# Optimization experiments

Hardware: AMD Instinct MI355X
Metric: run time of the kernel (lower is better)

Reference implementation:

```python
import jax, jax.numpy as jnp
import numpy as np

N, D, K, P, A = 16384, 256, 32, 64, 5
H, KD, NPT, FACT = 8, 32, 8, 2
RBF_BINS, RBF_MAX, REL_CLIP = 16, 10.0, 32


def _norm(v, eps=1e-6):
    return v * jax.lax.rsqrt(jnp.square(v).sum(-1, keepdims=True) + eps)


def extract_frames(pos):
    # pos: [N, A, 3]; backbone atoms 0=N, 1=CA, 2=C (Gram-Schmidt AF-style frame)
    n, ca, c = pos[:, 0], pos[:, 1], pos[:, 2]
    e1 = _norm(c - ca)
    u = n - ca
    e2 = _norm(u - (u * e1).sum(-1, keepdims=True) * e1)
    e3 = jnp.cross(e1, e2)
    R = jnp.stack([e1, e2, e3], axis=-1)  # [N,3,3], columns = frame axes
    t = ca
    local = jnp.einsum('nji,naj->nai', R, pos - t[:, None])  # R^T (p - t)
    return R, t, local


def distance_rbf(d):
    centers = jnp.linspace(0.0, RBF_MAX, RBF_BINS)
    sigma = RBF_MAX / RBF_BINS
    return jnp.exp(-jnp.square((d[..., None] - centers) / sigma))


def layer_norm(x, scale, offset, eps=1e-5):
    mu = x.mean(-1, keepdims=True)
    var = jnp.square(x - mu).mean(-1, keepdims=True)
    return (x - mu) * jax.lax.rsqrt(var + eps) * scale + offset


def setup_inputs() -> dict:
    key = jax.random.key(0)
    ks = jax.random.split(key, 20)
    f32 = jnp.float32
    rnd = lambda i, shape, s=0.02: jax.random.normal(ks[i], shape, f32) * s
    inp = {}
    inp['local'] = jax.random.normal(ks[0], (N, D), f32)
    inp['pos'] = jax.random.normal(ks[1], (N, A, 3), f32) * 3.0
    inp['neighbours'] = jax.random.randint(ks[2], (N, K), 0, N, jnp.int32)
    inp['resi'] = jnp.arange(N, dtype=jnp.int32) % 512
    inp['chain'] = jnp.arange(N, dtype=jnp.int32) // 2048
    inp['batch'] = jnp.arange(N, dtype=jnp.int32) // 4096
    inp['update_mask'] = jnp.ones((N, 1), bool)
    inp['mask'] = jnp.ones((N,), bool)
    FIN = A * 3 + A * RBF_BINS
    FPAIR = A * 3 + A * RBF_BINS + (2 * REL_CLIP + 1) + 2
    FOUT = H * KD + H * P + H * NPT * 3 + H * NPT
    inp['w_in'] = rnd(3, (FIN, D))
    inp['w_pair'] = rnd(4, (FPAIR, P))
    inp['b_pair'] = jnp.zeros((P,), f32)
    inp['ln1_s'] = jnp.ones((D,), f32); inp['ln1_o'] = jnp.zeros((D,), f32)
    inp['wq'] = rnd(5, (D, H * KD)); inp['wk'] = rnd(6, (D, H * KD)); inp['wv'] = rnd(7, (D, H * KD))
    inp['wqp'] = rnd(8, (D, H * NPT * 3)); inp['wkp'] = rnd(9, (D, H * NPT * 3)); inp['wvp'] = rnd(10, (D, H * NPT * 3))
    inp['wb'] = rnd(11, (P, H))
    inp['gamma'] = jnp.ones((H,), f32)
    inp['wo'] = rnd(12, (FOUT, D)); inp['bo'] = jnp.zeros((D,), f32)
    inp['ln2_s'] = jnp.ones((D,), f32); inp['ln2_o'] = jnp.zeros((D,), f32)
    DH = D * FACT
    inp['wg'] = rnd(13, (D, DH)); inp['wvm'] = rnd(14, (D, DH)); inp['wom'] = rnd(15, (DH, D))
    inp['ln3_s'] = jnp.ones((D,), f32); inp['ln3_o'] = jnp.zeros((D,), f32)
    inp['wpos'] = rnd(16, (D, A * 3))
    return inp


def reference(local, pos, w_in, w_pair, b_pair, ln1_s, ln1_o, wq, wk, wv, wqp, wkp, wvp,
              wb, gamma, wo, bo, ln2_s, ln2_o, wg, wvm, wom, ln3_s, ln3_o, wpos,
              neighbours, resi, chain, batch, update_mask, mask):
    n_res = local.shape[0]
    kk = neighbours.shape[1]
    R, t, local_pos = extract_frames(pos)  # [N,3,3], [N,3], [N,A,3]
    # --- geometric input features ---
    dloc = jnp.sqrt(jnp.square(local_pos).sum(-1) + 1e-12)
    feat = jnp.concatenate([_norm(local_pos).reshape(n_res, -1),
                            distance_rbf(dloc).reshape(n_res, -1)], axis=-1)
    local = local + feat @ w_in
    # --- pair features over kNN edges ---
    idx = jnp.clip(neighbours, 0, n_res - 1)
    pos_j = pos[idx]  # [N,K,A,3]
    rel = jnp.einsum('nji,nkaj->nkai', R, pos_j - t[:, None, None])  # neighbour atoms in frame i
    dij = jnp.sqrt(jnp.square(rel).sum(-1) + 1e-12)  # [N,K,A]
    dirs = rel / (dij[..., None] + 1e-6)
    rp = jnp.clip(resi[idx] - resi[:, None], -REL_CLIP, REL_CLIP) + REL_CLIP
    rp_oh = jax.nn.one_hot(rp, 2 * REL_CLIP + 1, dtype=local.dtype)
    same_chain = (chain[idx] == chain[:, None])[..., None].astype(local.dtype)
    same_batch = (batch[idx] == batch[:, None])[..., None].astype(local.dtype)
    pf = jnp.concatenate([dirs.reshape(n_res, kk, -1), distance_rbf(dij).reshape(n_res, kk, -1),
                          rp_oh, same_chain, same_batch], axis=-1)
    pair = jax.nn.gelu(pf @ w_pair + b_pair)  # [N,K,P]
    pair_mask = mask[:, None] & mask[idx] & (neighbours >= 0) & (batch[idx] == batch[:, None])
    # --- sparse invariant point attention ---
    x = layer_norm(local, ln1_s, ln1_o)
    q = (x @ wq).reshape(n_res, H, KD)
    k = (x @ wk).reshape(n_res, H, KD)
    v = (x @ wv).reshape(n_res, H, KD)
    to_glob = lambda pts: jnp.einsum('nij,nhpj->nhpi', R, pts) + t[:, None, None]
    qp = to_glob((x @ wqp).reshape(n_res, H, NPT, 3))
    kp = to_glob((x @ wkp).reshape(n_res, H, NPT, 3))
    vp = to_glob((x @ wvp).reshape(n_res, H, NPT, 3))
    qk = jnp.einsum('nhd,nkhd->nkh', q, k[idx]) / np.float32(np.sqrt(KD))
    d2 = jnp.square(qp[:, None] - kp[idx]).sum(-1).sum(-1)  # [N,K,H]
    wc = np.float32(np.sqrt(2.0 / (9.0 * NPT)))
    wl = np.float32(np.sqrt(1.0 / 3.0))
    logits = wl * (qk + pair @ wb - 0.5 * wc * jax.nn.softplus(gamma) * d2)
    logits = jnp.where(pair_mask[..., None], logits, -1e9)
    att = jax.nn.softmax(logits, axis=1)
    att = jnp.where(pair_mask[..., None], att, 0.0)
    o_s = jnp.einsum('nkh,nkhd->nhd', att, v[idx]).reshape(n_res, -1)
    o_pt = jnp.einsum('nkh,nkhpi->nhpi', att, vp[idx])
    o_pt = jnp.einsum('nji,nhpj->nhpi', R, o_pt - t[:, None, None])  # back to local frame
    o_n = jnp.sqrt(jnp.square(o_pt).sum(-1) + 1e-8)
    o_pr = jnp.einsum('nkh,nkc->nhc', att, pair).reshape(n_res, -1)
    ipa = jnp.concatenate([o_s, o_pr, o_pt.reshape(n_res, -1), o_n.reshape(n_res, -1)], -1) @ wo + bo
    local = local + ipa
    # --- gated MLP ---
    x = layer_norm(local, ln2_s, ln2_o)
    local = local + (jax.nn.gelu(x @ wg) * (x @ wvm)) @ wom
    # --- equivariant position update (scale = 1.0) ---
    x = layer_norm(local, ln3_s, ln3_o)
    new_lp = local_pos + (x @ wpos).reshape(n_res, A, 3)
    new_pos = jnp.einsum('nij,naj->nai', R, new_lp) + t[:, None]
    pos = jnp.where(update_mask[..., None], new_pos, pos)
    return local, pos
```

## Files before the change

### kernel.cpp

```cpp
#include <hip/hip_runtime.h>
#include <hip/hip_bf16.h>
#include <math.h>

#define DMODEL 256
#define KNB 32
#define NHEAD 8
#define FIN 95
#define FPD 95
#define KPAD 104
#define FOUT 1024
#define DHID 512

typedef __hip_bfloat16 bf16;
typedef __attribute__((ext_vector_type(8))) short short8;
typedef __attribute__((ext_vector_type(4))) float floatx4;

__device__ inline float B2F(bf16 x) { return __bfloat162float(x); }
__device__ inline bf16 F2B(float x) { return __float2bfloat16(x); }
__device__ inline unsigned short f2bs(float x) {
    bf16 h = __float2bfloat16(x);
    return *reinterpret_cast<unsigned short*>(&h);
}
__device__ inline float bs2f(short s) {
    return __uint_as_float(((unsigned)(unsigned short)s) << 16);
}

__device__ inline float gelu_t(float x) {
    return 0.5f * x * (1.f + tanhf(0.7978845608028654f * (x + 0.044715f * x * x * x)));
}

#define OFF_WALL 0
#define OFF_WO   344064
#define OFF_WG   606208
#define OFF_WVM  737280
#define OFF_WOM  868352
#define OFF_WP   999424
#define OFF_WIN  1006080
#define WT_TOTAL 1032704

__global__ __launch_bounds__(256) void kT(const float* __restrict__ wq, const float* __restrict__ wk,
                                          const float* __restrict__ wv, const float* __restrict__ wqp,
                                          const float* __restrict__ wkp, const float* __restrict__ wvp,
                                          const float* __restrict__ wo, const float* __restrict__ wg,
                                          const float* __restrict__ wvm, const float* __restrict__ wom,
                                          const float* __restrict__ w_pair, const float* __restrict__ w_in,
                                          unsigned short* __restrict__ wt) {
    int stride = gridDim.x * 256;
    for (int e = blockIdx.x * 256 + threadIdx.x; e < WT_TOTAL; e += stride) {
        float v;
        if (e < OFF_WO) {
            int n = e >> 8, k = e & 255;
            if (n < 256) v = wq[k * 256 + n];
            else if (n < 512) v = wk[k * 256 + n - 256];
            else if (n < 768) v = wv[k * 256 + n - 512];
            else if (n < 960) v = wqp[k * 192 + n - 768];
            else if (n < 1152) v = wkp[k * 192 + n - 960];
            else v = wvp[k * 192 + n - 1152];
        } else if (e < OFF_WG) {
            int u = e - OFF_WO; int n = u >> 10, k = u & 1023;
            v = wo[k * 256 + n];
        } else if (e < OFF_WVM) {
            int u = e - OFF_WG; int n = u >> 8, k = u & 255;
            v = wg[k * 512 + n];
        } else if (e < OFF_WOM) {
            int u = e - OFF_WVM; int n = u >> 8, k = u & 255;
            v = wvm[k * 512 + n];
        } else if (e < OFF_WP) {
            int u = e - OFF_WOM; int n = u >> 9, k = u & 511;
            v = wom[k * 256 + n];
        } else if (e < OFF_WIN) {
            int u = e - OFF_WP; int n = u / KPAD, k = u % KPAD;
            v = (k < FPD) ? w_pair[k * 64 + n] : 0.f;
        } else {
            int u = e - OFF_WIN; int n = u / KPAD, k = u % KPAD;
            v = (k < FIN) ? w_in[k * 256 + n] : 0.f;
        }
        wt[e] = f2bs(v);
    }
}

__global__ __launch_bounds__(256) void kA1(const float* __restrict__ pos,
                                           float* __restrict__ Rw,
                                           float* __restrict__ lpw,
                                           unsigned short* __restrict__ featb) {
    int tid = threadIdx.x;
    int res = tid >> 5, lt = tid & 31;
    int ri = blockIdx.x * 8 + res;
    const float* pp = pos + (size_t)ri * 15;
    float nx = pp[0], ny = pp[1], nz = pp[2];
    float cax = pp[3], cay = pp[4], caz = pp[5];
    float cx = pp[6], cy = pp[7], cz = pp[8];
    float e1x = cx - cax, e1y = cy - cay, e1z = cz - caz;
    float inv = rsqrtf(e1x * e1x + e1y * e1y + e1z * e1z + 1e-6f);
    e1x *= inv; e1y *= inv; e1z *= inv;
    float ux = nx - cax, uy = ny - cay, uz = nz - caz;
    float d = ux * e1x + uy * e1y + uz * e1z;
    float wx = ux - d * e1x, wy = uy - d * e1y, wz = uz - d * e1z;
    inv = rsqrtf(wx * wx + wy * wy + wz * wz + 1e-6f);
    float e2x = wx * inv, e2y = wy * inv, e2z = wz * inv;
    float e3x = e1y * e2z - e1z * e2y;
    float e3y = e1z * e2x - e1x * e2z;
    float e3z = e1x * e2y - e1y * e2x;
    float R[9] = {e1x, e2x, e3x, e1y, e2y, e3y, e1z, e2z, e3z};

    __shared__ float lpS[8][15];
    __shared__ float ddS[8][5], dinvS[8][5];

    if (lt < 9) Rw[(size_t)ri * 9 + lt] = R[lt];
    if (lt < 15) {
        int a = lt / 3, ii = lt % 3;
        float px = pp[a * 3 + 0] - cax, py = pp[a * 3 + 1] - cay, pz = pp[a * 3 + 2] - caz;
        float v = R[0 * 3 + ii] * px + R[1 * 3 + ii] * py + R[2 * 3 + ii] * pz;
        lpS[res][lt] = v;
        lpw[(size_t)ri * 15 + lt] = v;
    }
    __syncthreads();
    if (lt < 5) {
        float s = lpS[res][lt * 3] * lpS[res][lt * 3] + lpS[res][lt * 3 + 1] * lpS[res][lt * 3 + 1] +
                  lpS[res][lt * 3 + 2] * lpS[res][lt * 3 + 2];
        ddS[res][lt] = sqrtf(s + 1e-12f);
        dinvS[res][lt] = rsqrtf(s + 1e-6f);
    }
    __syncthreads();
    for (int e = lt; e < KPAD; e += 32) {
        float v;
        if (e < 15) v = lpS[res][e] * dinvS[res][e / 3];
        else if (e < 95) {
            int u = e - 15, a = u >> 4, b = u & 15;
            float z = (ddS[res][a] - (float)b * (10.f / 15.f)) * (1.f / 0.625f);
            v = expf(-z * z);
        } else v = 0.f;
        featb[(size_t)ri * KPAD + e] = f2bs(v);
    }
}

__global__ __launch_bounds__(256) void kB(const float* __restrict__ local,
                                          const unsigned short* __restrict__ featb,
                                          const float* __restrict__ ln1_s,
                                          const float* __restrict__ ln1_o,
                                          const unsigned short* __restrict__ wAllT,
                                          const unsigned short* __restrict__ w_inT,
                                          float* __restrict__ dlocal,
                                          bf16* __restrict__ qbh, bf16* __restrict__ kvb,
                                          bf16* __restrict__ qpl, bf16* __restrict__ kpl,
                                          bf16* __restrict__ vpl) {
    int r0 = blockIdx.x * 32;
    int tid = threadIdx.x;
    __shared__ __align__(16) unsigned short featA[32 * KPAD];
    __shared__ __align__(16) unsigned short xbf[32 * 264];
    __shared__ float statsS[32 * 4];

    {
        const short8* src = reinterpret_cast<const short8*>(featb + (size_t)r0 * KPAD);
        short8* dst = reinterpret_cast<short8*>(featA);
        for (int c = tid; c < 32 * KPAD / 8; c += 256) dst[c] = src[c];
    }
    __syncthreads();

    int lane = tid & 63, w = tid >> 6;
    int mtile = w & 1, par = w >> 1;
    int m = lane & 15, quad = lane >> 4;

    short8 fa[3];
#pragma unroll
    for (int ks = 0; ks < 3; ks++)
        fa[ks] = *reinterpret_cast<const short8*>(&featA[(mtile * 16 + m) * KPAD + ks * 32 + quad * 8]);
    float lupv[8][4];
#pragma unroll
    for (int j = 0; j < 8; j++) {
        int nt = par + 2 * j;
        floatx4 c = {0.f, 0.f, 0.f, 0.f};
        const short8* bp = reinterpret_cast<const short8*>(w_inT + (size_t)(nt * 16 + m) * KPAD);
#pragma unroll
        for (int ks = 0; ks < 3; ks++)
            c = __builtin_amdgcn_mfma_f32_16x16x32_bf16(fa[ks], bp[ks * 4 + quad], c, 0, 0, 0);
        int col = nt * 16 + m;
#pragma unroll
        for (int r = 0; r < 4; r++) {
            int row = mtile * 16 + quad * 4 + r;
            float lv = local[(size_t)(r0 + row) * 256 + col] + c[r];
            lupv[j][r] = lv;
            dlocal[(size_t)(r0 + row) * 256 + col] = lv;
        }
    }
    {
        float s[4] = {0.f, 0.f, 0.f, 0.f}, ss[4] = {0.f, 0.f, 0.f, 0.f};
#pragma unroll
        for (int j = 0; j < 8; j++)
#pragma unroll
            for (int r = 0; r < 4; r++) { s[r] += lupv[j][r]; ss[r] += lupv[j][r] * lupv[j][r]; }
#pragma unroll
        for (int mask = 1; mask < 16; mask <<= 1)
#pragma unroll
            for (int r = 0; r < 4; r++) { s[r] += __shfl_xor(s[r], mask); ss[r] += __shfl_xor(ss[r], mask); }
        if (m == 0) {
#pragma unroll
            for (int r = 0; r < 4; r++) {
                int row = mtile * 16 + quad * 4 + r;
                statsS[row * 4 + par * 2 + 0] = s[r];
                statsS[row * 4 + par * 2 + 1] = ss[r];
            }
        }
    }
    __syncthreads();
    {
        float mu[4], rs_[4];
#pragma unroll
        for (int r = 0; r < 4; r++) {
            int row = mtile * 16 + quad * 4 + r;
            float S = statsS[row * 4 + 0] + statsS[row * 4 + 2];
            float SS = statsS[row * 4 + 1] + statsS[row * 4 + 3];
            float m_ = S * (1.f / 256.f);
            mu[r] = m_;
            rs_[r] = rsqrtf(SS * (1.f / 256.f) - m_ * m_ + 1e-5f);
        }
#pragma unroll
        for (int j = 0; j < 8; j++) {
            int col = (par + 2 * j) * 16 + m;
            float g = ln1_s[col], o = ln1_o[col];
#pragma unroll
            for (int r = 0; r < 4; r++) {
                int row = mtile * 16 + quad * 4 + r;
                xbf[row * 264 + col] = f2bs((lupv[j][r] - mu[r]) * rs_[r] * g + o);
            }
        }
    }
    __syncthreads();

    short8 afr[8];
#pragma unroll
    for (int ks = 0; ks < 8; ks++)
        afr[ks] = *reinterpret_cast<const short8*>(&xbf[(mtile * 16 + m) * 264 + ks * 32 + quad * 8]);
    for (int nt = par; nt < 84; nt += 2) {
        floatx4 c = {0.f, 0.f, 0.f, 0.f};
        const short8* bp = reinterpret_cast<const short8*>(wAllT + (size_t)(nt * 16 + m) * 256);
#pragma unroll
        for (int ks = 0; ks < 8; ks++)
            c = __builtin_amdgcn_mfma_f32_16x16x32_bf16(afr[ks], bp[ks * 4 + quad], c, 0, 0, 0);
        int colg = nt * 16 + m;
        bf16* O; int c0, ncol;
        if (colg < 256)       { O = qbh; c0 = colg;        ncol = 256; }
        else if (colg < 768)  { O = kvb; c0 = colg - 256;  ncol = 512; }
        else if (colg < 960)  { O = qpl; c0 = colg - 768;  ncol = 192; }
        else if (colg < 1152) { O = kpl; c0 = colg - 960;  ncol = 192; }
        else                  { O = vpl; c0 = colg - 1152; ncol = 192; }
#pragma unroll
        for (int r = 0; r < 4; r++) {
            int rg = r0 + mtile * 16 + quad * 4 + r;
            O[(size_t)rg * ncol + c0] = F2B(c[r]);
        }
    }
}

__global__ __launch_bounds__(256) void kP(const bf16* __restrict__ qpl,
                                          const bf16* __restrict__ kpl,
                                          const bf16* __restrict__ vpl,
                                          const float* __restrict__ Rw,
                                          const float* __restrict__ pos,
                                          float* __restrict__ qpg,
                                          float* __restrict__ kvpg) {
    int r0 = blockIdx.x * 4;
    int tid = threadIdx.x;
    for (int u = tid; u < 4 * 192; u += 256) {
        int r = u / 192, e = u % 192, hp = e / 3, ii = e % 3;
        int ri = r0 + r;
        float R0 = Rw[(size_t)ri * 9 + ii * 3 + 0];
        float R1 = Rw[(size_t)ri * 9 + ii * 3 + 1];
        float R2 = Rw[(size_t)ri * 9 + ii * 3 + 2];
        float tt = pos[(size_t)ri * 15 + 3 + ii];
        size_t base = (size_t)ri * 192 + hp * 3;
        qpg[(size_t)ri * 192 + e] = R0 * B2F(qpl[base]) + R1 * B2F(qpl[base + 1]) + R2 * B2F(qpl[base + 2]) + tt;
        kvpg[(size_t)ri * 384 + e] = R0 * B2F(kpl[base]) + R1 * B2F(kpl[base + 1]) + R2 * B2F(kpl[base + 2]) + tt;
        kvpg[(size_t)ri * 384 + 192 + e] = R0 * B2F(vpl[base]) + R1 * B2F(vpl[base + 1]) + R2 * B2F(vpl[base + 2]) + tt;
    }
}

__global__ __launch_bounds__(256) void kC(const float* __restrict__ pos,
                                          const int* __restrict__ nbr,
                                          const int* __restrict__ resi,
                                          const int* __restrict__ chain,
                                          const int* __restrict__ batch,
                                          const int* __restrict__ mask,
                                          const float* __restrict__ Rw,
                                          const float* __restrict__ w_pair,
                                          const unsigned short* __restrict__ wT,
                                          const float* __restrict__ b_pair,
                                          const float* __restrict__ wbm,
                                          const float* __restrict__ gamma,
                                          const bf16* __restrict__ qbh,
                                          const bf16* __restrict__ kvb,
                                          const float* __restrict__ qpg,
                                          const float* __restrict__ kvpg,
                                          bf16* __restrict__ ipab,
                                          int N) {
    int i = blockIdx.x;
    int tid = threadIdx.x;
    __shared__ __align__(16) float qS[256];
    __shared__ __align__(16) float qpS[192];
    __shared__ __align__(16) unsigned short pfA[KNB * KPAD];
    __shared__ __align__(16) float pairS[KNB][68];
    __shared__ __align__(16) float wbmS[NHEAD][68];
    __shared__ float spS[NHEAD];
    __shared__ float lg[KNB * NHEAD];
    __shared__ float optg[192];
    __shared__ float ipaS[FOUT];
    __shared__ int idxS[KNB], rpS[KNB], scS[KNB], sbS[KNB], pmS[KNB];

    float R[9];
#pragma unroll
    for (int u = 0; u < 9; u++) R[u] = Rw[(size_t)i * 9 + u];
    float t0 = pos[(size_t)i * 15 + 3];
    float t1 = pos[(size_t)i * 15 + 4];
    float t2 = pos[(size_t)i * 15 + 5];

    qS[tid] = B2F(qbh[(size_t)i * 256 + tid]);
    if (tid < 192) qpS[tid] = qpg[(size_t)i * 192 + tid];
    if (tid < KNB) {
        int nb = nbr[(size_t)i * KNB + tid];
        int j = min(max(nb, 0), N - 1);
        idxS[tid] = j;
        int rp = resi[j] - resi[i];
        rp = min(max(rp, -32), 32) + 32;
        rpS[tid] = rp;
        scS[tid] = (chain[j] == chain[i]) ? 1 : 0;
        sbS[tid] = (batch[j] == batch[i]) ? 1 : 0;
        pmS[tid] = (mask[i] != 0 && mask[j] != 0 && nb >= 0 && batch[j] == batch[i]) ? 1 : 0;
    }
    __syncthreads();
    for (int u = tid; u < 512; u += 256) {
        int h = u & 7, c = u >> 3;
        wbmS[h][c] = wbm[c * 8 + h];
    }
    if (tid >= 192 && tid < 200) spS[tid - 192] = log1pf(expf(gamma[tid - 192]));
    if (tid < 160) {
        int kk = tid & 31, a = tid >> 5;
        int j = idxS[kk];
        const float* pj = pos + (size_t)j * 15 + a * 3;
        float px = pj[0] - t0, py = pj[1] - t1, pz = pj[2] - t2;
        float r0_ = R[0] * px + R[3] * py + R[6] * pz;
        float r1_ = R[1] * px + R[4] * py + R[7] * pz;
        float r2_ = R[2] * px + R[5] * py + R[8] * pz;
        float s = r0_ * r0_ + r1_ * r1_ + r2_ * r2_;
        float dij = sqrtf(s + 1e-12f);
        float di = 1.f / (dij + 1e-6f);
        pfA[kk * KPAD + a * 3 + 0] = f2bs(r0_ * di);
        pfA[kk * KPAD + a * 3 + 1] = f2bs(r1_ * di);
        pfA[kk * KPAD + a * 3 + 2] = f2bs(r2_ * di);
        for (int b = 0; b < 16; b++) {
            float z = (dij - (float)b * (10.f / 15.f)) * (1.f / 0.625f);
            pfA[kk * KPAD + 15 + a * 16 + b] = f2bs(expf(-z * z));
        }
    }
    if (tid < KNB) pfA[tid * KPAD + FPD] = 0;
    __syncthreads();

    {
        int lane = tid & 63;
        int wv = tid >> 6;
        int n0 = wv * 16;
        int mrow = lane & 15;
        int quad = lane >> 4;
        floatx4 c0 = {0.f, 0.f, 0.f, 0.f};
        floatx4 c1 = {0.f, 0.f, 0.f, 0.f};
#pragma unroll
        for (int ks = 0; ks < 3; ks++) {
            int k0 = ks * 32 + quad * 8;
            short8 a0 = *reinterpret_cast<const short8*>(&pfA[mrow * KPAD + k0]);
            short8 a1 = *reinterpret_cast<const short8*>(&pfA[(16 + mrow) * KPAD + k0]);
            short8 bb = *reinterpret_cast<const short8*>(&wT[(n0 + mrow) * KPAD + k0]);
            c0 = __builtin_amdgcn_mfma_f32_16x16x32_bf16(a0, bb, c0, 0, 0, 0);
            c1 = __builtin_amdgcn_mfma_f32_16x16x32_bf16(a1, bb, c1, 0, 0, 0);
        }
        int col = n0 + mrow;
        float bp = b_pair[col];
        float w160 = w_pair[160 * 64 + col];
        float w161 = w_pair[161 * 64 + col];
#pragma unroll
        for (int mt = 0; mt < 2; mt++) {
            floatx4 cc = mt ? c1 : c0;
#pragma unroll
            for (int r = 0; r < 4; r++) {
                int row = mt * 16 + quad * 4 + r;
                float s = cc[r] + bp + w_pair[(95 + rpS[row]) * 64 + col] +
                          (scS[row] ? w160 : 0.f) + (sbS[row] ? w161 : 0.f);
                pairS[row][col] = gelu_t(s);
            }
        }
    }
    __syncthreads();

    {
        int kk = tid >> 3, h = tid & 7;
        int j = idxS[kk];
        float qk = 0.f;
        const short8* kj8 = reinterpret_cast<const short8*>(kvb + (size_t)j * 512 + h * 32);
        const floatx4* qh4 = reinterpret_cast<const floatx4*>(qS + h * 32);
#pragma unroll
        for (int e = 0; e < 4; e++) {
            short8 kv = kj8[e];
            floatx4 qa = qh4[2 * e], qb = qh4[2 * e + 1];
            qk += qa[0] * bs2f(kv[0]) + qa[1] * bs2f(kv[1]) + qa[2] * bs2f(kv[2]) + qa[3] * bs2f(kv[3]) +
                  qb[0] * bs2f(kv[4]) + qb[1] * bs2f(kv[5]) + qb[2] * bs2f(kv[6]) + qb[3] * bs2f(kv[7]);
        }
        qk *= 0.17677669529663687f;
        float d2 = 0.f;
        const floatx4* kp4 = reinterpret_cast<const floatx4*>(kvpg + (size_t)j * 384 + h * 24);
        const floatx4* qp4 = reinterpret_cast<const floatx4*>(qpS + h * 24);
#pragma unroll
        for (int e = 0; e < 6; e++) {
            floatx4 kv = kp4[e], qv = qp4[e];
#pragma unroll
            for (int q = 0; q < 4; q++) {
                float df = qv[q] - kv[q];
                d2 += df * df;
            }
        }
        float pb = 0.f;
        const floatx4* ps4 = reinterpret_cast<const floatx4*>(&pairS[kk][0]);
        const floatx4* wb4 = reinterpret_cast<const floatx4*>(&wbmS[h][0]);
#pragma unroll
        for (int e = 0; e < 16; e++) {
            floatx4 pv = ps4[e], wv4 = wb4[e];
            pb += pv[0] * wv4[0] + pv[1] * wv4[1] + pv[2] * wv4[2] + pv[3] * wv4[3];
        }
        float lgt = 0.5773502691896258f * (qk + pb - (1.f / 12.f) * spS[h] * d2);
        lg[kk * 8 + h] = pmS[kk] ? lgt : -1e9f;
    }
    __syncthreads();
    if (tid < 64) {
        int h = tid >> 3, sub = tid & 7;
        float m = -INFINITY;
        float lv[4];
#pragma unroll
        for (int q = 0; q < 4; q++) {
            lv[q] = lg[(sub + 8 * q) * 8 + h];
            m = fmaxf(m, lv[q]);
        }
#pragma unroll
        for (int mk = 1; mk < 8; mk <<= 1) m = fmaxf(m, __shfl_xor(m, mk));
        float s = 0.f, ex[4];
#pragma unroll
        for (int q = 0; q < 4; q++) { ex[q] = expf(lv[q] - m); s += ex[q]; }
#pragma unroll
        for (int mk = 1; mk < 8; mk <<= 1) s += __shfl_xor(s, mk);
        float invs = 1.f / s;
#pragma unroll
        for (int q = 0; q < 4; q++) {
            int kk = sub + 8 * q;
            lg[kk * 8 + h] = pmS[kk] ? ex[q] * invs : 0.f;
        }
    }
    __syncthreads();
    {
        int h = tid >> 5, d = tid & 31;
        float s = 0.f;
        for (int kk = 0; kk < KNB; kk++)
            s += lg[kk * 8 + h] * B2F(kvb[(size_t)idxS[kk] * 512 + 256 + h * 32 + d]);
        ipaS[h * 32 + d] = s;
    }
    for (int u = tid; u < 512; u += 256) {
        int h = u >> 6, c = u & 63;
        float s = 0.f;
        for (int kk = 0; kk < KNB; kk++) s += lg[kk * 8 + h] * pairS[kk][c];
        ipaS[256 + u] = s;
    }
    if (tid < 192) {
        int h = tid / 24;
        float s = 0.f;
        for (int kk = 0; kk < KNB; kk++)
            s += lg[kk * 8 + h] * kvpg[(size_t)idxS[kk] * 384 + 192 + tid];
        optg[tid] = s;
    }
    __syncthreads();
    if (tid < 192) {
        int hp = tid / 3, ii = tid % 3;
        float v0 = optg[hp * 3 + 0] - t0, v1 = optg[hp * 3 + 1] - t1, v2 = optg[hp * 3 + 2] - t2;
        ipaS[768 + tid] = R[0 + ii] * v0 + R[3 + ii] * v1 + R[6 + ii] * v2;
    }
    __syncthreads();
    if (tid < 64) {
        float a0 = ipaS[768 + tid * 3], a1 = ipaS[768 + tid * 3 + 1], a2 = ipaS[768 + tid * 3 + 2];
        ipaS[960 + tid] = sqrtf(a0 * a0 + a1 * a1 + a2 * a2 + 1e-8f);
    }
    __syncthreads();
    for (int u = tid; u < FOUT; u += 256) ipab[(size_t)i * FOUT + u] = F2B(ipaS[u]);
}

__global__ __launch_bounds__(256) void kDE(const bf16* __restrict__ ipab,
                                           const unsigned short* __restrict__ woT,
                                           const float* __restrict__ bo,
                                           const float* __restrict__ ln2_s,
                                           const float* __restrict__ ln2_o,
                                           const unsigned short* __restrict__ wgT,
                                           const unsigned short* __restrict__ wvmT,
                                           const unsigned short* __restrict__ womT,
                                           float* __restrict__ dlocal) {
    int r0 = blockIdx.x * 32;
    int tid = threadIdx.x;
    __shared__ __align__(16) unsigned short xbf[32 * 264];
    __shared__ __align__(16) unsigned short hbf[32 * 520];
    __shared__ float statsS[32 * 4];
    int lane = tid & 63, w = tid >> 6;
    int mtile = w & 1, par = w >> 1, m = lane & 15, quad = lane >> 4;

    floatx4 l2[8];
#pragma unroll
    for (int j = 0; j < 8; j++) l2[j] = {0.f, 0.f, 0.f, 0.f};
    const short8* arow = reinterpret_cast<const short8*>(ipab + (size_t)(r0 + mtile * 16 + m) * 1024);
    for (int ks = 0; ks < 32; ks++) {
        short8 a = arow[ks * 4 + quad];
#pragma unroll
        for (int j = 0; j < 8; j++) {
            int nt = par + 2 * j;
            const short8* bp = reinterpret_cast<const short8*>(woT + (size_t)(nt * 16 + m) * 1024);
            l2[j] = __builtin_amdgcn_mfma_f32_16x16x32_bf16(a, bp[ks * 4 + quad], l2[j], 0, 0, 0);
        }
    }
#pragma unroll
    for (int j = 0; j < 8; j++) {
        int colg = (par + 2 * j) * 16 + m;
        float bov = bo[colg];
#pragma unroll
        for (int r = 0; r < 4; r++) {
            int row = mtile * 16 + quad * 4 + r;
            l2[j][r] += dlocal[(size_t)(r0 + row) * 256 + colg] + bov;
        }
    }
    {
        float s[4] = {0.f, 0.f, 0.f, 0.f}, ss[4] = {0.f, 0.f, 0.f, 0.f};
#pragma unroll
        for (int j = 0; j < 8; j++)
#pragma unroll
            for (int r = 0; r < 4; r++) { s[r] += l2[j][r]; ss[r] += l2[j][r] * l2[j][r]; }
#pragma unroll
        for (int mask = 1; mask < 16; mask <<= 1)
#pragma unroll
            for (int r = 0; r < 4; r++) { s[r] += __shfl_xor(s[r], mask); ss[r] += __shfl_xor(ss[r], mask); }
        if (m == 0) {
#pragma unroll
            for (int r = 0; r < 4; r++) {
                int row = mtile * 16 + quad * 4 + r;
                statsS[row * 4 + par * 2 + 0] = s[r];
                statsS[row * 4 + par * 2 + 1] = ss[r];
            }
        }
    }
    __syncthreads();
    {
        float mu[4], rs_[4];
#pragma unroll
        for (int r = 0; r < 4; r++) {
            int row = mtile * 16 + quad * 4 + r;
            float S = statsS[row * 4 + 0] + statsS[row * 4 + 2];
            float SS = statsS[row * 4 + 1] + statsS[row * 4 + 3];
            float m_ = S * (1.f / 256.f);
            mu[r] = m_;
            rs_[r] = rsqrtf(SS * (1.f / 256.f) - m_ * m_ + 1e-5f);
        }
#pragma unroll
        for (int j = 0; j < 8; j++) {
            int colg = (par + 2 * j) * 16 + m;
            float g = ln2_s[colg], o = ln2_o[colg];
#pragma unroll
            for (int r = 0; r < 4; r++) {
                int row = mtile * 16 + quad * 4 + r;
                xbf[row * 264 + colg] = f2bs((l2[j][r] - mu[r]) * rs_[r] * g + o);
            }
        }
    }
    __syncthreads();
    short8 afr[8];
#pragma unroll
    for (int ks = 0; ks < 8; ks++)
        afr[ks] = *reinterpret_cast<const short8*>(&xbf[(mtile * 16 + m) * 264 + ks * 32 + quad * 8]);
    for (int nt = par; nt < 32; nt += 2) {
        floatx4 cg = {0.f, 0.f, 0.f, 0.f};
        floatx4 cv = {0.f, 0.f, 0.f, 0.f};
        const short8* bg = reinterpret_cast<const short8*>(wgT + (size_t)(nt * 16 + m) * 256);
        const short8* bv = reinterpret_cast<const short8*>(wvmT + (size_t)(nt * 16 + m) * 256);
#pragma unroll
        for (int ks = 0; ks < 8; ks++) {
            cg = __builtin_amdgcn_mfma_f32_16x16x32_bf16(afr[ks], bg[ks * 4 + quad], cg, 0, 0, 0);
            cv = __builtin_amdgcn_mfma_f32_16x16x32_bf16(afr[ks], bv[ks * 4 + quad], cv, 0, 0, 0);
        }
#pragma unroll
        for (int r = 0; r < 4; r++) {
            int row = mtile * 16 + quad * 4 + r;
            hbf[row * 520 + nt * 16 + m] = f2bs(gelu_t(cg[r]) * cv[r]);
        }
    }
    __syncthreads();
    floatx4 acc[8];
#pragma unroll
    for (int j = 0; j < 8; j++) acc[j] = {0.f, 0.f, 0.f, 0.f};
    for (int ks = 0; ks < 16; ks++) {
        short8 a = *reinterpret_cast<const short8*>(&hbf[(mtile * 16 + m) * 520 + ks * 32 + quad * 8]);
#pragma unroll
        for (int j = 0; j < 8; j++) {
            int nt = par + 2 * j;
            const short8* bp = reinterpret_cast<const short8*>(womT + (size_t)(nt * 16 + m) * 512);
            acc[j] = __builtin_amdgcn_mfma_f32_16x16x32_bf16(a, bp[ks * 4 + quad], acc[j], 0, 0, 0);
        }
    }
#pragma unroll
    for (int j = 0; j < 8; j++) {
        int colg = (par + 2 * j) * 16 + m;
#pragma unroll
        for (int r = 0; r < 4; r++) {
            int row = mtile * 16 + quad * 4 + r;
            dlocal[(size_t)(r0 + row) * 256 + colg] = l2[j][r] + acc[j][r];
        }
    }
}

__global__ __launch_bounds__(256) void kF(const float* __restrict__ dlocal,
                                          const float* __restrict__ ln3_s,
                                          const float* __restrict__ ln3_o,
                                          const float* __restrict__ wpos,
                                          const float* __restrict__ lpw,
                                          const float* __restrict__ Rw,
                                          const float* __restrict__ pos,
                                          const int* __restrict__ umask,
                                          float* __restrict__ outp) {
    int tid = threadIdx.x;
    int r = tid >> 5, lt = tid & 31;
    int ri = blockIdx.x * 8 + r;
    __shared__ float x3S[8][256];
    __shared__ float nlS[8][15];
    {
        const floatx4* src = reinterpret_cast<const floatx4*>(dlocal + (size_t)ri * 256 + lt * 8);
        floatx4 v0 = src[0], v1 = src[1];
        float s = 0.f, ss = 0.f;
#pragma unroll
        for (int q = 0; q < 4; q++) {
            s += v0[q] + v1[q];
            ss += v0[q] * v0[q] + v1[q] * v1[q];
        }
#pragma unroll
        for (int mask = 1; mask < 32; mask <<= 1) { s += __shfl_xor(s, mask); ss += __shfl_xor(ss, mask); }
        float mu = s * (1.f / 256.f);
        float var = ss * (1.f / 256.f) - mu * mu;
        float rs = rsqrtf(var + 1e-5f);
#pragma unroll
        for (int q = 0; q < 4; q++) {
            int f0 = lt * 8 + q, f1 = lt * 8 + 4 + q;
            x3S[r][f0] = (v0[q] - mu) * rs * ln3_s[f0] + ln3_o[f0];
            x3S[r][f1] = (v1[q] - mu) * rs * ln3_s[f1] + ln3_o[f1];
        }
    }
    __syncthreads();
    {
        int g = tid >> 5, sub = tid & 31;
        for (int out = g; out < 120; out += 8) {
            int rr = out / 15, e = out % 15;
            float partial = 0.f;
#pragma unroll
            for (int i2 = 0; i2 < 8; i2++) {
                int f = sub + 32 * i2;
                partial += x3S[rr][f] * wpos[f * 15 + e];
            }
#pragma unroll
            for (int mask = 1; mask < 32; mask <<= 1) partial += __shfl_xor(partial, mask);
            if (sub == 0) nlS[rr][e] = lpw[(size_t)(blockIdx.x * 8 + rr) * 15 + e] + partial;
        }
    }
    __syncthreads();
    if (tid < 120) {
        int rr = tid / 15, e = tid % 15;
        int rj = blockIdx.x * 8 + rr;
        int a2 = e / 3, ii = e % 3;
        float R0 = Rw[(size_t)rj * 9 + ii * 3 + 0];
        float R1 = Rw[(size_t)rj * 9 + ii * 3 + 1];
        float R2 = Rw[(size_t)rj * 9 + ii * 3 + 2];
        float tt = pos[(size_t)rj * 15 + 3 + ii];
        float np = R0 * nlS[rr][a2 * 3 + 0] + R1 * nlS[rr][a2 * 3 + 1] + R2 * nlS[rr][a2 * 3 + 2] + tt;
        float old = pos[(size_t)rj * 15 + e];
        outp[(size_t)rj * 15 + e] = (umask[rj] != 0) ? np : old;
    }
}

extern "C" void kernel_launch(void* const* d_in, const int* in_sizes, int n_in,
                              void* d_out, int out_size, void* d_ws, size_t ws_size,
                              hipStream_t stream) {
    static const int map_dict[31] = {0, 1, 2, 3, 4, 5, 6, 7, 8, 9, 10, 11, 12, 13, 14, 15,
                                     16, 17, 18, 19, 20, 21, 22, 23, 24, 25, 26, 27, 28, 29, 30};
    static const int map_sig[31] = {0, 1, 25, 26, 27, 28, 29, 30, 2, 3, 4, 5, 6, 7, 8, 9,
                                    10, 11, 12, 13, 14, 15, 16, 17, 18, 19, 20, 21, 22, 23, 24};
    const int* M = (in_sizes[2] == FIN * DMODEL) ? map_sig : map_dict;

    const float* local = (const float*)d_in[M[0]];
    const float* pos = (const float*)d_in[M[1]];
    const int* nbr = (const int*)d_in[M[2]];
    const int* resi = (const int*)d_in[M[3]];
    const int* chain = (const int*)d_in[M[4]];
    const int* batch = (const int*)d_in[M[5]];
    const int* umask = (const int*)d_in[M[6]];
    const int* mask = (const int*)d_in[M[7]];
    const float* w_in = (const float*)d_in[M[8]];
    const float* w_pair = (const float*)d_in[M[9]];
    const float* b_pair = (const float*)d_in[M[10]];
    const float* ln1_s = (const float*)d_in[M[11]];
    const float* ln1_o = (const float*)d_in[M[12]];
    const float* wq = (const float*)d_in[M[13]];
    const float* wk = (const float*)d_in[M[14]];
    const float* wv = (const float*)d_in[M[15]];
    const float* wqp = (const float*)d_in[M[16]];
    const float* wkp = (const float*)d_in[M[17]];
    const float* wvp = (const float*)d_in[M[18]];
    const float* wbm = (const float*)d_in[M[19]];
    const float* gamma = (const float*)d_in[M[20]];
    const float* wo = (const float*)d_in[M[21]];
    const float* bo = (const float*)d_in[M[22]];
    const float* ln2_s = (const float*)d_in[M[23]];
    const float* ln2_o = (const float*)d_in[M[24]];
    const float* wg = (const float*)d_in[M[25]];
    const float* wvm = (const float*)d_in[M[26]];
    const float* wom = (const float*)d_in[M[27]];
    const float* ln3_s = (const float*)d_in[M[28]];
    const float* ln3_o = (const float*)d_in[M[29]];
    const float* wpos = (const float*)d_in[M[30]];

    int N = in_sizes[0] / DMODEL;

    float* out_local = (float*)d_out;
    float* out_pos = out_local + (size_t)N * DMODEL;

    char* wsb = (char*)d_ws;
    float* Rw = (float*)wsb;   wsb += (size_t)N * 9 * 4;
    float* lpw = (float*)wsb;  wsb += (size_t)N * 15 * 4;
    bf16* qbh = (bf16*)wsb;    wsb += (size_t)N * 256 * 2;
    bf16* kvb = (bf16*)wsb;    wsb += (size_t)N * 512 * 2;
    bf16* qpl = (bf16*)wsb;    wsb += (size_t)N * 192 * 2;
    bf16* kpl = (bf16*)wsb;    wsb += (size_t)N * 192 * 2;
    bf16* vpl = (bf16*)wsb;    wsb += (size_t)N * 192 * 2;
    bf16* ipab = (bf16*)wsb;   wsb += (size_t)N * 1024 * 2;
    float* qpg = (float*)wsb;  wsb += (size_t)N * 192 * 4;
    float* kvpg = (float*)wsb; wsb += (size_t)N * 384 * 4;
    unsigned short* featb = (unsigned short*)wsb; wsb += (size_t)N * KPAD * 2;
    unsigned short* wtrans = (unsigned short*)wsb; wsb += (size_t)WT_TOTAL * 2;
    unsigned short* wAllT = wtrans + OFF_WALL;
    unsigned short* woT   = wtrans + OFF_WO;
    unsigned short* wgT   = wtrans + OFF_WG;
    unsigned short* wvmT  = wtrans + OFF_WVM;
    unsigned short* womT  = wtrans + OFF_WOM;
    unsigned short* wpT   = wtrans + OFF_WP;
    unsigned short* winT  = wtrans + OFF_WIN;

    dim3 blk(256);
    hipLaunchKernelGGL(kT, dim3(512), blk, 0, stream, wq, wk, wv, wqp, wkp, wvp,
                       wo, wg, wvm, wom, w_pair, w_in, wtrans);
    hipLaunchKernelGGL(kA1, dim3(N / 8), blk, 0, stream, pos, Rw, lpw, featb);
    hipLaunchKernelGGL(kB, dim3(N / 32), blk, 0, stream, local, featb, ln1_s, ln1_o, wAllT, winT,
                       out_local, qbh, kvb, qpl, kpl, vpl);
    hipLaunchKernelGGL(kP, dim3(N / 4), blk, 0, stream, qpl, kpl, vpl, Rw, pos, qpg, kvpg);
    hipLaunchKernelGGL(kC, dim3(N), blk, 0, stream, pos, nbr, resi, chain, batch, mask, Rw,
                       w_pair, wpT, b_pair, wbm, gamma, qbh, kvb, qpg, kvpg, ipab, N);
    hipLaunchKernelGGL(kDE, dim3(N / 32), blk, 0, stream, ipab, woT, bo, ln2_s, ln2_o,
                       wgT, wvmT, womT, out_local);
    hipLaunchKernelGGL(kF, dim3(N / 8), blk, 0, stream, out_local, ln3_s, ln3_o, wpos, lpw, Rw, pos,
                       umask, out_pos);
}
```

Baseline: 673.7 us.

## Use MFMA for attention aggregation and pair bias in IPA kernel

The per-residue attention kernel now stages neighbour values, centred value points and pair features transposed in shared memory as bf16. The attention-weighted sums over neighbours and the pair-bias projection become MFMA matrix multiplies instead of scalar loops over global memory. It also swaps in faster exp/gelu approximations, reuses shared buffers through a union, and adds a bf16 copy of wb to the weight-transpose kernel. This lowers precision for the value aggregation and adds LDS transpose traffic and a correction for the all-masked case.

```diff
diff --git a/kernel.cpp b/kernel.cpp
--- a/kernel.cpp
+++ b/kernel.cpp
@@ -10,6 +10,8 @@
 #define KPAD 104
 #define FOUT 1024
 #define DHID 512
+#define BTS 36
+#define PRS 72
 
 typedef __hip_bfloat16 bf16;
 typedef __attribute__((ext_vector_type(8))) short short8;
@@ -27,6 +29,12 @@
 
 __device__ inline float gelu_t(float x) {
     return 0.5f * x * (1.f + tanhf(0.7978845608028654f * (x + 0.044715f * x * x * x)));
+}
+
+__device__ inline float gelu_f(float x) {
+    float u = 1.5957691216057308f * x * (1.f + 0.044715f * x * x);
+    float t = 1.f - 2.f / (1.f + __expf(u));
+    return 0.5f * x * (1.f + t);
 }
 
 #define OFF_WALL 0
@@ -36,7 +44,8 @@
 #define OFF_WOM  868352
 #define OFF_WP   999424
 #define OFF_WIN  1006080
-#define WT_TOTAL 1032704
+#define OFF_WBM  1032704
+#define WT_TOTAL 1033728
 
 __global__ __launch_bounds__(256) void kT(const float* __restrict__ wq, const float* __restrict__ wk,
                                           const float* __restrict__ wv, const float* __restrict__ wqp,
@@ -44,6 +53,7 @@
                                           const float* __restrict__ wo, const float* __restrict__ wg,
                                           const float* __restrict__ wvm, const float* __restrict__ wom,
                                           const float* __restrict__ w_pair, const float* __restrict__ w_in,
+                                          const float* __restrict__ wbm,
                                           unsigned short* __restrict__ wt) {
     int stride = gridDim.x * 256;
     for (int e = blockIdx.x * 256 + threadIdx.x; e < WT_TOTAL; e += stride) {
@@ -71,9 +81,12 @@
         } else if (e < OFF_WIN) {
             int u = e - OFF_WP; int n = u / KPAD, k = u % KPAD;
             v = (k < FPD) ? w_pair[k * 64 + n] : 0.f;
-        } else {
+        } else if (e < OFF_WBM) {
             int u = e - OFF_WIN; int n = u / KPAD, k = u % KPAD;
             v = (k < FIN) ? w_in[k * 256 + n] : 0.f;
+        } else {
+            int u = e - OFF_WBM; int n = u >> 6, k = u & 63;
+            v = (n < NHEAD) ? wbm[k * 8 + n] : 0.f;
         }
         wt[e] = f2bs(v);
     }
@@ -285,7 +298,7 @@
                                           const float* __restrict__ w_pair,
                                           const unsigned short* __restrict__ wT,
                                           const float* __restrict__ b_pair,
-                                          const float* __restrict__ wbm,
+                                          const unsigned short* __restrict__ wbmT,
                                           const float* __restrict__ gamma,
                                           const bf16* __restrict__ qbh,
                                           const bf16* __restrict__ kvb,
@@ -295,16 +308,19 @@
                                           int N) {
     int i = blockIdx.x;
     int tid = threadIdx.x;
+    __shared__ __align__(16) unsigned short BigT[512 * BTS];
+    __shared__ __align__(16) unsigned short pairR[32 * PRS];
+    __shared__ __align__(16) unsigned short attb[16 * 40];
     __shared__ __align__(16) float qS[256];
     __shared__ __align__(16) float qpS[192];
-    __shared__ __align__(16) unsigned short pfA[KNB * KPAD];
-    __shared__ __align__(16) float pairS[KNB][68];
-    __shared__ __align__(16) float wbmS[NHEAD][68];
+    __shared__ __align__(16) float pbS[256];
     __shared__ float spS[NHEAD];
-    __shared__ float lg[KNB * NHEAD];
-    __shared__ float optg[192];
-    __shared__ float ipaS[FOUT];
+    __shared__ int anyS;
     __shared__ int idxS[KNB], rpS[KNB], scS[KNB], sbS[KNB], pmS[KNB];
+    __shared__ __align__(16) union UShare {
+        unsigned short pfA[32 * KPAD];
+        struct { float ipaS[FOUT]; float optg[192]; } o;
+    } uS;
 
     float R[9];
 #pragma unroll
@@ -315,6 +331,7 @@
 
     qS[tid] = B2F(qbh[(size_t)i * 256 + tid]);
     if (tid < 192) qpS[tid] = qpg[(size_t)i * 192 + tid];
+    if (tid < NHEAD) spS[tid] = log1pf(expf(gamma[tid]));
     if (tid < KNB) {
         int nb = nbr[(size_t)i * KNB + tid];
         int j = min(max(nb, 0), N - 1);
@@ -327,11 +344,10 @@
         pmS[tid] = (mask[i] != 0 && mask[j] != 0 && nb >= 0 && batch[j] == batch[i]) ? 1 : 0;
     }
     __syncthreads();
-    for (int u = tid; u < 512; u += 256) {
-        int h = u & 7, c = u >> 3;
-        wbmS[h][c] = wbm[c * 8 + h];
-    }
-    if (tid >= 192 && tid < 200) spS[tid - 192] = log1pf(expf(gamma[tid - 192]));
+    if (tid < 64) {
+        unsigned long long b = __ballot((tid < KNB) && (pmS[tid] != 0));
+        if (tid == 0) anyS = (b != 0ULL) ? 1 : 0;
+    }
     if (tid < 160) {
         int kk = tid & 31, a = tid >> 5;
         int j = idxS[kk];
@@ -343,15 +359,15 @@
         float s = r0_ * r0_ + r1_ * r1_ + r2_ * r2_;
         float dij = sqrtf(s + 1e-12f);
         float di = 1.f / (dij + 1e-6f);
-        pfA[kk * KPAD + a * 3 + 0] = f2bs(r0_ * di);
-        pfA[kk * KPAD + a * 3 + 1] = f2bs(r1_ * di);
-        pfA[kk * KPAD + a * 3 + 2] = f2bs(r2_ * di);
+        uS.pfA[kk * KPAD + a * 3 + 0] = f2bs(r0_ * di);
+        uS.pfA[kk * KPAD + a * 3 + 1] = f2bs(r1_ * di);
+        uS.pfA[kk * KPAD + a * 3 + 2] = f2bs(r2_ * di);
         for (int b = 0; b < 16; b++) {
             float z = (dij - (float)b * (10.f / 15.f)) * (1.f / 0.625f);
-            pfA[kk * KPAD + 15 + a * 16 + b] = f2bs(expf(-z * z));
-        }
-    }
-    if (tid < KNB) pfA[tid * KPAD + FPD] = 0;
+            uS.pfA[kk * KPAD + 15 + a * 16 + b] = f2bs(__expf(-z * z));
+        }
+    }
+    if (tid < KNB) uS.pfA[tid * KPAD + FPD] = 0;
     __syncthreads();
 
     {
@@ -365,8 +381,8 @@
 #pragma unroll
         for (int ks = 0; ks < 3; ks++) {
             int k0 = ks * 32 + quad * 8;
-            short8 a0 = *reinterpret_cast<const short8*>(&pfA[mrow * KPAD + k0]);
-            short8 a1 = *reinterpret_cast<const short8*>(&pfA[(16 + mrow) * KPAD + k0]);
+            short8 a0 = *reinterpret_cast<const short8*>(&uS.pfA[mrow * KPAD + k0]);
+            short8 a1 = *reinterpret_cast<const short8*>(&uS.pfA[(16 + mrow) * KPAD + k0]);
             short8 bb = *reinterpret_cast<const short8*>(&wT[(n0 + mrow) * KPAD + k0]);
             c0 = __builtin_amdgcn_mfma_f32_16x16x32_bf16(a0, bb, c0, 0, 0, 0);
             c1 = __builtin_amdgcn_mfma_f32_16x16x32_bf16(a1, bb, c1, 0, 0, 0);
@@ -383,7 +399,60 @@
                 int row = mt * 16 + quad * 4 + r;
                 float s = cc[r] + bp + w_pair[(95 + rpS[row]) * 64 + col] +
                           (scS[row] ? w160 : 0.f) + (sbS[row] ? w161 : 0.f);
-                pairS[row][col] = gelu_t(s);
+                unsigned short gb = f2bs(gelu_f(s));
+                pairR[row * PRS + col] = gb;
+                BigT[(448 + col) * BTS + row] = gb;
+            }
+        }
+    }
+    __syncthreads();
+
+    {
+        int kk = tid & 31, seg = tid >> 5;
+        int j = idxS[kk];
+        {
+            const short8* src = reinterpret_cast<const short8*>(kvb + (size_t)j * 512 + 256 + seg * 32);
+            short8 v0 = src[0], v1 = src[1], v2 = src[2], v3 = src[3];
+#pragma unroll
+            for (int c = 0; c < 8; c++) BigT[(seg * 32 + c) * BTS + kk] = (unsigned short)v0[c];
+#pragma unroll
+            for (int c = 0; c < 8; c++) BigT[(seg * 32 + 8 + c) * BTS + kk] = (unsigned short)v1[c];
+#pragma unroll
+            for (int c = 0; c < 8; c++) BigT[(seg * 32 + 16 + c) * BTS + kk] = (unsigned short)v2[c];
+#pragma unroll
+            for (int c = 0; c < 8; c++) BigT[(seg * 32 + 24 + c) * BTS + kk] = (unsigned short)v3[c];
+        }
+        {
+            const floatx4* src = reinterpret_cast<const floatx4*>(kvpg + (size_t)j * 384 + 192 + seg * 24);
+            floatx4 f[6];
+#pragma unroll
+            for (int g = 0; g < 6; g++) f[g] = src[g];
+            float tv[3] = {t0, t1, t2};
+#pragma unroll
+            for (int g = 0; g < 6; g++)
+#pragma unroll
+                for (int c2 = 0; c2 < 4; c2++) {
+                    int x = g * 4 + c2;
+                    float val = f[g][c2] - tv[x % 3];
+                    BigT[(256 + seg * 24 + x) * BTS + kk] = f2bs(val);
+                }
+        }
+    }
+    {
+        int w = tid >> 6;
+        if (w < 2) {
+            int lane = tid & 63, la = lane & 15, quad = lane >> 4;
+            floatx4 c = {0.f, 0.f, 0.f, 0.f};
+#pragma unroll
+            for (int ks = 0; ks < 2; ks++) {
+                short8 a = *reinterpret_cast<const short8*>(&pairR[(w * 16 + la) * PRS + ks * 32 + quad * 8]);
+                short8 b = *reinterpret_cast<const short8*>(wbmT + la * 64 + ks * 32 + quad * 8);
+                c = __builtin_amdgcn_mfma_f32_16x16x32_bf16(a, b, c, 0, 0, 0);
+            }
+            if (la < NHEAD) {
+#pragma unroll
+                for (int r = 0; r < 4; r++)
+                    pbS[(w * 16 + quad * 4 + r) * 8 + la] = c[r];
             }
         }
     }
@@ -415,75 +484,95 @@
                 d2 += df * df;
             }
         }
-        float pb = 0.f;
-        const floatx4* ps4 = reinterpret_cast<const floatx4*>(&pairS[kk][0]);
-        const floatx4* wb4 = reinterpret_cast<const floatx4*>(&wbmS[h][0]);
-#pragma unroll
-        for (int e = 0; e < 16; e++) {
-            floatx4 pv = ps4[e], wv4 = wb4[e];
-            pb += pv[0] * wv4[0] + pv[1] * wv4[1] + pv[2] * wv4[2] + pv[3] * wv4[3];
-        }
+        float pb = pbS[kk * 8 + h];
         float lgt = 0.5773502691896258f * (qk + pb - (1.f / 12.f) * spS[h] * d2);
-        lg[kk * 8 + h] = pmS[kk] ? lgt : -1e9f;
-    }
-    __syncthreads();
+        pbS[kk * 8 + h] = pmS[kk] ? lgt : -1e9f;
+    }
+    __syncthreads();
+
     if (tid < 64) {
         int h = tid >> 3, sub = tid & 7;
         float m = -INFINITY;
         float lv[4];
 #pragma unroll
         for (int q = 0; q < 4; q++) {
-            lv[q] = lg[(sub + 8 * q) * 8 + h];
+            lv[q] = pbS[(sub + 8 * q) * 8 + h];
             m = fmaxf(m, lv[q]);
         }
 #pragma unroll
         for (int mk = 1; mk < 8; mk <<= 1) m = fmaxf(m, __shfl_xor(m, mk));
         float s = 0.f, ex[4];
 #pragma unroll
-        for (int q = 0; q < 4; q++) { ex[q] = expf(lv[q] - m); s += ex[q]; }
+        for (int q = 0; q < 4; q++) { ex[q] = __expf(lv[q] - m); s += ex[q]; }
 #pragma unroll
         for (int mk = 1; mk < 8; mk <<= 1) s += __shfl_xor(s, mk);
         float invs = 1.f / s;
 #pragma unroll
         for (int q = 0; q < 4; q++) {
             int kk = sub + 8 * q;
-            lg[kk * 8 + h] = pmS[kk] ? ex[q] * invs : 0.f;
-        }
-    }
-    __syncthreads();
-    {
-        int h = tid >> 5, d = tid & 31;
-        float s = 0.f;
-        for (int kk = 0; kk < KNB; kk++)
-            s += lg[kk * 8 + h] * B2F(kvb[(size_t)idxS[kk] * 512 + 256 + h * 32 + d]);
-        ipaS[h * 32 + d] = s;
-    }
-    for (int u = tid; u < 512; u += 256) {
-        int h = u >> 6, c = u & 63;
-        float s = 0.f;
-        for (int kk = 0; kk < KNB; kk++) s += lg[kk * 8 + h] * pairS[kk][c];
-        ipaS[256 + u] = s;
-    }
-    if (tid < 192) {
-        int h = tid / 24;
-        float s = 0.f;
-        for (int kk = 0; kk < KNB; kk++)
-            s += lg[kk * 8 + h] * kvpg[(size_t)idxS[kk] * 384 + 192 + tid];
-        optg[tid] = s;
-    }
-    __syncthreads();
+            float a = pmS[kk] ? ex[q] * invs : 0.f;
+            attb[h * 40 + kk] = f2bs(a);
+        }
+    } else if (tid < 128) {
+        int t2 = tid - 64;
+        int h2 = 8 + (t2 >> 3);
+        int k0 = (t2 & 7) * 4;
+#pragma unroll
+        for (int q = 0; q < 4; q++) attb[h2 * 40 + k0 + q] = 0;
+    }
+    __syncthreads();
+
+    {
+        int lane = tid & 63, w = tid >> 6;
+        int la = lane & 15, quad = lane >> 4;
+        short8 af = *reinterpret_cast<const short8*>(&attb[la * 40 + quad * 8]);
+        float* oB = uS.o.ipaS;
+#pragma unroll
+        for (int n8 = 0; n8 < 8; n8++) {
+            int nt = w * 8 + n8;
+            int colg = nt * 16 + la;
+            union { short8 s; unsigned long long u[2]; } bb;
+            const unsigned long long* bp = reinterpret_cast<const unsigned long long*>(&BigT[colg * BTS + quad * 8]);
+            bb.u[0] = bp[0]; bb.u[1] = bp[1];
+            floatx4 z = {0.f, 0.f, 0.f, 0.f};
+            floatx4 d = __builtin_amdgcn_mfma_f32_16x16x32_bf16(af, bb.s, z, 0, 0, 0);
+            if (quad < 2) {
+                if (colg < 448) {
+                    int h_req, dst;
+                    if (colg < 256) { h_req = colg >> 5; dst = (h_req << 5) + (colg & 31); }
+                    else            { int e = colg - 256; h_req = e / 24; dst = 1024 + e; }
+                    if ((h_req >> 2) == quad) {
+#pragma unroll
+                        for (int r = 0; r < 4; r++)
+                            if ((h_req & 3) == r) oB[dst] = d[r];
+                    }
+                } else {
+                    int c = colg - 448;
+#pragma unroll
+                    for (int r = 0; r < 4; r++)
+                        oB[256 + (quad * 4 + r) * 64 + c] = d[r];
+                }
+            }
+        }
+    }
+    __syncthreads();
+
     if (tid < 192) {
         int hp = tid / 3, ii = tid % 3;
-        float v0 = optg[hp * 3 + 0] - t0, v1 = optg[hp * 3 + 1] - t1, v2 = optg[hp * 3 + 2] - t2;
-        ipaS[768 + tid] = R[0 + ii] * v0 + R[3 + ii] * v1 + R[6 + ii] * v2;
+        float corr = anyS ? 0.f : -1.f;
+        const float* optg = uS.o.ipaS + 1024;
+        float v0 = optg[hp * 3 + 0] + corr * t0;
+        float v1 = optg[hp * 3 + 1] + corr * t1;
+        float v2 = optg[hp * 3 + 2] + corr * t2;
+        uS.o.ipaS[768 + tid] = R[0 + ii] * v0 + R[3 + ii] * v1 + R[6 + ii] * v2;
     }
     __syncthreads();
     if (tid < 64) {
-        float a0 = ipaS[768 + tid * 3], a1 = ipaS[768 + tid * 3 + 1], a2 = ipaS[768 + tid * 3 + 2];
-        ipaS[960 + tid] = sqrtf(a0 * a0 + a1 * a1 + a2 * a2 + 1e-8f);
-    }
-    __syncthreads();
-    for (int u = tid; u < FOUT; u += 256) ipab[(size_t)i * FOUT + u] = F2B(ipaS[u]);
+        float a0 = uS.o.ipaS[768 + tid * 3], a1 = uS.o.ipaS[768 + tid * 3 + 1], a2 = uS.o.ipaS[768 + tid * 3 + 2];
+        uS.o.ipaS[960 + tid] = sqrtf(a0 * a0 + a1 * a1 + a2 * a2 + 1e-8f);
+    }
+    __syncthreads();
+    for (int u = tid; u < FOUT; u += 256) ipab[(size_t)i * FOUT + u] = F2B(uS.o.ipaS[u]);
 }
 
 __global__ __launch_bounds__(256) void kDE(const bf16* __restrict__ ipab,
@@ -745,16 +834,17 @@
     unsigned short* womT  = wtrans + OFF_WOM;
     unsigned short* wpT   = wtrans + OFF_WP;
     unsigned short* winT  = wtrans + OFF_WIN;
+    unsigned short* wbmT  = wtrans + OFF_WBM;
 
     dim3 blk(256);
     hipLaunchKernelGGL(kT, dim3(512), blk, 0, stream, wq, wk, wv, wqp, wkp, wvp,
-                       wo, wg, wvm, wom, w_pair, w_in, wtrans);
+                       wo, wg, wvm, wom, w_pair, w_in, wbm, wtrans);
     hipLaunchKernelGGL(kA1, dim3(N / 8), blk, 0, stream, pos, Rw, lpw, featb);
     hipLaunchKernelGGL(kB, dim3(N / 32), blk, 0, stream, local, featb, ln1_s, ln1_o, wAllT, winT,
                        out_local, qbh, kvb, qpl, kpl, vpl);
     hipLaunchKernelGGL(kP, dim3(N / 4), blk, 0, stream, qpl, kpl, vpl, Rw, pos, qpg, kvpg);
     hipLaunchKernelGGL(kC, dim3(N), blk, 0, stream, pos, nbr, resi, chain, batch, mask, Rw,
-                       w_pair, wpT, b_pair, wbm, gamma, qbh, kvb, qpg, kvpg, ipab, N);
+                       w_pair, wpT, b_pair, wbmT, gamma, qbh, kvb, qpg, kvpg, ipab, N);
     hipLaunchKernelGGL(kDE, dim3(N / 32), blk, 0, stream, ipab, woT, bo, ln2_s, ln2_o,
                        wgT, wvmT, womT, out_local);
     hipLaunchKernelGGL(kF, dim3(N / 8), blk, 0, stream, out_local, ln3_s, ln3_o, wpos, lpw, Rw, pos,
```

Result: slower. 702.7 us (+4.3%).
